# Optimization experiments

Measured on AMD Instinct MI355X. Metric: run time of the kernel, lower is better.

The kernel has to match this reference:

```python
import jax, jax.numpy as jnp
import numpy as np

VOCAB, EMB = 100000, 50
KERNEL_NUM, SIGMA, EXACT_SIGMA = 21, 0.1, 0.001
OUT_LAYERS = [10, 5]


def _kernel_params():
    # Mirrors KNRM._get_kernels_layers
    mus = [1.0]
    bin_size = 2.0 / (KERNEL_NUM - 1)
    mus.append(1 - bin_size / 2)
    for i in range(1, KERNEL_NUM - 1):
        mus.append(mus[i] - bin_size)
    mus = list(reversed(mus))
    sigmas = [SIGMA] * (KERNEL_NUM - 1) + [EXACT_SIGMA]
    return np.array(mus, np.float32), np.array(sigmas, np.float32)

MUS, SIGMAS = _kernel_params()


def setup_inputs() -> dict:
    key = jax.random.key(0)
    ks = jax.random.split(key, 12)
    B, LQ, LD = 2048, 32, 256
    emb = jax.random.normal(ks[0], (VOCAB, EMB), jnp.float32)
    emb = emb.at[0].set(0.0)  # padding_idx=0
    query1 = jax.random.randint(ks[1], (B, LQ), 0, VOCAB)
    doc1 = jax.random.randint(ks[2], (B, LD), 0, VOCAB)
    query2 = jax.random.randint(ks[3], (B, LQ), 0, VOCAB)
    doc2 = jax.random.randint(ks[4], (B, LD), 0, VOCAB)
    def lin(k, fan_in, fan_out):
        bound = 1.0 / np.sqrt(fan_in)
        kw, kb = jax.random.split(k)
        w = jax.random.uniform(kw, (fan_out, fan_in), jnp.float32, -bound, bound)
        b = jax.random.uniform(kb, (fan_out,), jnp.float32, -bound, bound)
        return w, b
    w0, b0 = lin(ks[5], KERNEL_NUM, OUT_LAYERS[0])
    w1, b1 = lin(ks[6], OUT_LAYERS[0], OUT_LAYERS[1])
    w2, b2 = lin(ks[7], OUT_LAYERS[1], 1)
    return dict(emb=emb, w0=w0, b0=b0, w1=w1, b1=b1, w2=w2, b2=b2,
                query1=query1, doc1=doc1, query2=query2, doc2=doc2)


def _matching_matrix(emb, query, doc):
    qe = emb[query]                     # [B, Lq, E]
    de = emb[doc]                       # [B, Ld, E]
    qn = qe / (jnp.linalg.norm(qe, axis=-1, keepdims=True) + 1e-13)
    dn = de / (jnp.linalg.norm(de, axis=-1, keepdims=True) + 1e-13)
    return jnp.einsum('bqe,bde->bqd', qn, dn)  # cosine sim [B, Lq, Ld]


def _apply_kernels(mm):
    # Loop over the fixed 21 kernels (structurally distinct mu/sigma),
    # avoiding a [B,Lq,Ld,21] intermediate, as the original does.
    km = []
    for mu, sg in zip(MUS, SIGMAS):
        k = jnp.exp(-(mm - mu) ** 2 / (2.0 * sg * sg))
        km.append(jnp.log1p(k.sum(axis=-1)).sum(axis=-1))  # [B]
    return jnp.stack(km, axis=1)  # [B, K]


def _mlp(x, w0, b0, w1, b1, w2, b2):
    h = jax.nn.relu(x @ w0.T + b0)
    h = jax.nn.relu(h @ w1.T + b1)
    return h @ w2.T + b2  # [B, 1]


def _predict(emb, w0, b0, w1, b1, w2, b2, query, doc):
    mm = _matching_matrix(emb, query, doc)
    ko = _apply_kernels(mm)
    return _mlp(ko, w0, b0, w1, b1, w2, b2)


def reference(emb, w0, b0, w1, b1, w2, b2, query1, doc1, query2, doc2):
    logits1 = _predict(emb, w0, b0, w1, b1, w2, b2, query1, doc1)
    logits2 = _predict(emb, w0, b0, w1, b1, w2, b2, query2, doc2)
    return jax.nn.sigmoid(logits1 - logits2)  # [B, 1]
```

## Files before the change

### kernel.cpp

```cpp
#include <hip/hip_runtime.h>

#define EMB_N 50
#define KP 64
#define LQ 32
#define LD 256
#define KN 21
#define BATCH 2048

typedef short v8s __attribute__((ext_vector_type(8)));
typedef float v4f __attribute__((ext_vector_type(4)));
typedef float v2f __attribute__((ext_vector_type(2)));

#define PK_ACC(d, b)    asm("v_pk_add_f32 %0, %0, %1" : "+v"(d) : "v"(b))
#define PK_MULA(d, b)   asm("v_pk_mul_f32 %0, %0, %1" : "+v"(d) : "v"(b))

__device__ inline short bf16_rne(float f) {
  unsigned u = __float_as_uint(f);
  unsigned r = u + 0x7fffu + ((u >> 16) & 1u);
  return (short)(r >> 16);
}
__device__ inline float bf16_tof(short h) {
  return __uint_as_float(((unsigned)(unsigned short)h) << 16);
}

__global__ __launch_bounds__(256) void vocab_norm_kernel(
    const float* __restrict__ emb, short* __restrict__ vb,
    short* __restrict__ vlo, int vocab)
{
  int gid = blockIdx.x * 256 + threadIdx.x;
  int r = gid >> 3;
  int c = gid & 7;
  if (r >= vocab) return;
  const float* row = emb + (size_t)r * EMB_N;
  float v[8];
#pragma unroll
  for (int k = 0; k < 8; k++) v[k] = 0.f;
  float ss = 0.f;
  int e0 = c * 8;
  if (c < 6) {
    const float2* p = (const float2*)(row + e0);
#pragma unroll
    for (int k = 0; k < 4; k++) {
      float2 t = p[k];
      v[2*k] = t.x; v[2*k+1] = t.y;
      ss = fmaf(t.x, t.x, ss); ss = fmaf(t.y, t.y, ss);
    }
  } else if (c == 6) {
    float2 t = *(const float2*)(row + 48);
    v[0] = t.x; v[1] = t.y;
    ss = fmaf(t.x, t.x, t.y * t.y);
  }
  ss += __shfl_xor(ss, 1);
  ss += __shfl_xor(ss, 2);
  ss += __shfl_xor(ss, 4);
  float inv = 1.0f / (sqrtf(ss) + 1e-13f);
  short hi[8], lo[8];
#pragma unroll
  for (int k = 0; k < 8; k++) {
    float f = v[k] * inv;
    hi[k] = bf16_rne(f);
    lo[k] = bf16_rne(f - bf16_tof(hi[k]));
  }
  size_t o = (size_t)r * KP + e0;
  *(uint4*)(vb + o)  = *(const uint4*)hi;
  *(uint4*)(vlo + o) = *(const uint4*)lo;
}

__device__ __constant__ const float CJ[KN] = {
  2.5261639e-20f, 2.0469719e-16f, 6.1019363e-13f, 6.6915861e-10f, 2.6995785e-7f,
  4.0065297e-5f,  2.1874911e-3f,  4.3936937e-2f,  0.32465247f,    0.88249690f,
  0.88249690f,    0.32465247f,    4.3936937e-2f,  2.1874911e-3f,  4.0065297e-5f,
  2.6995785e-7f,  6.6915861e-10f, 6.1019363e-13f, 2.0469719e-16f, 2.5261639e-20f,
  1.0f
};

__global__ __launch_bounds__(256, 6) void knrm_main_kernel(
    const short* __restrict__ vb, const short* __restrict__ vlo,
    const int* __restrict__ q1, const int* __restrict__ d1,
    const int* __restrict__ q2, const int* __restrict__ d2,
    const float* __restrict__ w0, const float* __restrict__ b0,
    const float* __restrict__ w1, const float* __restrict__ b1,
    const float* __restrict__ w2, const float* __restrict__ b2,
    float* __restrict__ lgbuf)
{
  __shared__ float part[4][16][KN];
  __shared__ float Sqex[LQ];
  __shared__ float ko[KN];
  __shared__ float h0s[10];
  __shared__ float h1s[5];

  const int pair = blockIdx.x >> 11;
  const int b = blockIdx.x & (BATCH - 1);
  const int tid = threadIdx.x;
  const int wave = tid >> 6;
  const int lane = tid & 63;
  const int l15 = lane & 15;
  const int quad = lane >> 4;
  const int qtile = wave >> 1;
  const int thalf = wave & 1;

  const int* qp = pair ? q2 : q1;
  const int* dp = pair ? d2 : d1;

  if (tid < LQ) Sqex[tid] = 0.f;

  int qtok = qp[b * LQ + qtile * 16 + l15];
  const short* qh = vb  + (size_t)qtok * KP + quad * 8;
  const short* ql = vlo + (size_t)qtok * KP + quad * 8;
  v8s Bh0 = *(const v8s*)(qh);
  v8s Bh1 = *(const v8s*)(qh + 32);
  v8s Bl0 = *(const v8s*)(ql);
  v8s Bl1 = *(const v8s*)(ql + 32);

  int mydtok = dp[b * LD + tid];

  __syncthreads();

#pragma unroll
  for (int qq = 0; qq < LQ; qq++) {
    int qt = qp[b * LQ + qq];
    unsigned long long m = __ballot(mydtok == qt && qt != 0);
    if (lane == 0 && m)
      atomicAdd(&Sqex[qq], (float)__popcll(m));
  }

  v2f U2[10];
#pragma unroll
  for (int i = 0; i < 10; i++) U2[i] = (v2f){0.f, 0.f};

#pragma unroll 1
  for (int t = 0; t < 8; t++) {
    int dtok = dp[b * LD + (thalf * 8 + t) * 16 + l15];
    const short* dptr = vb + (size_t)dtok * KP + quad * 8;
    v8s A0 = *(const v8s*)(dptr);
    v8s A1 = *(const v8s*)(dptr + 32);

    v4f C = {0.f, 0.f, 0.f, 0.f};
    C = __builtin_amdgcn_mfma_f32_16x16x32_bf16(A0, Bh0, C, 0, 0, 0);
    C = __builtin_amdgcn_mfma_f32_16x16x32_bf16(A1, Bh1, C, 0, 0, 0);
    C = __builtin_amdgcn_mfma_f32_16x16x32_bf16(A0, Bl0, C, 0, 0, 0);
    C = __builtin_amdgcn_mfma_f32_16x16x32_bf16(A1, Bl1, C, 0, 0, 0);

#pragma unroll
    for (int rp = 0; rp < 2; rp++) {
      v2f p0, p1, rr0, rr1;
      {
        float x = C[rp * 2];
        float gc = __builtin_amdgcn_exp2f(x * fmaf(-72.1347520f, x, 7.2134752f));
        float ex = 14.4269504f * x;
        float e1 = __builtin_amdgcn_exp2f(ex);
        float ei = __builtin_amdgcn_exp2f(-ex);
        p0 = (v2f){gc, gc * ei};  rr0 = (v2f){e1, ei};
      }
      {
        float x = C[rp * 2 + 1];
        float gc = __builtin_amdgcn_exp2f(x * fmaf(-72.1347520f, x, 7.2134752f));
        float ex = 14.4269504f * x;
        float e1 = __builtin_amdgcn_exp2f(ex);
        float ei = __builtin_amdgcn_exp2f(-ex);
        p1 = (v2f){gc, gc * ei};  rr1 = (v2f){e1, ei};
      }
#pragma unroll
      for (int k2 = 0; k2 < 10; k2++) {
        PK_ACC(U2[k2], p0);
        PK_MULA(p0, rr0);
        PK_ACC(U2[k2], p1);
        PK_MULA(p1, rr1);
      }
    }
  }

#pragma unroll
  for (int i = 0; i < 10; i++) {
    float ux = U2[i].x, uy = U2[i].y;
    ux += __shfl_xor(ux, 16);  uy += __shfl_xor(uy, 16);
    ux += __shfl_xor(ux, 32);  uy += __shfl_xor(uy, 32);
    if (quad == 0) {
      part[wave][l15][10 + i] = ux;
      part[wave][l15][9 - i]  = uy;
    }
  }
  __syncthreads();

  {
    int qq = tid & 31;
    int qi = qq & 15, qt2 = qq >> 4;
    int jb = tid >> 5;
#pragma unroll
    for (int k = 0; k < 3; k++) {
      int j = jb + 8 * k;
      float l = 0.f;
      if (j < KN) {
        float s = (j < 20) ? part[qt2 * 2][qi][j] + part[qt2 * 2 + 1][qi][j]
                           : Sqex[qq];
        float y = fmaf(CJ[j], s, 1.0f);
        l = 0.69314718f * __builtin_amdgcn_logf(y);
      }
      l += __shfl_xor(l, 1);  l += __shfl_xor(l, 2);
      l += __shfl_xor(l, 4);  l += __shfl_xor(l, 8);
      l += __shfl_xor(l, 16);
      if (qq == 0 && j < KN) ko[j] = l;
    }
  }
  __syncthreads();

  if (tid < 10) {
    float h = b0[tid];
#pragma unroll
    for (int k = 0; k < KN; k++) h = fmaf(w0[tid * KN + k], ko[k], h);
    h0s[tid] = fmaxf(h, 0.f);
  }
  __syncthreads();
  if (tid < 5) {
    float h = b1[tid];
#pragma unroll
    for (int k = 0; k < 10; k++) h = fmaf(w1[tid * 10 + k], h0s[k], h);
    h1s[tid] = fmaxf(h, 0.f);
  }
  __syncthreads();
  if (tid == 0) {
    float h = b2[0];
#pragma unroll
    for (int k = 0; k < 5; k++) h = fmaf(w2[k], h1s[k], h);
    lgbuf[pair * BATCH + b] = h;
  }
}

__global__ __launch_bounds__(256) void knrm_combine_kernel(
    const float* __restrict__ lgbuf, float* __restrict__ out)
{
  int i = blockIdx.x * 256 + threadIdx.x;
  if (i < BATCH) {
    float z = lgbuf[i] - lgbuf[BATCH + i];
    out[i] = 1.0f / (1.0f + expf(-z));
  }
}

extern "C" void kernel_launch(void* const* d_in, const int* in_sizes, int n_in,
                              void* d_out, int out_size, void* d_ws, size_t ws_size,
                              hipStream_t stream)
{
  const float* emb = (const float*)d_in[0];
  const float* w0  = (const float*)d_in[1];
  const float* b0  = (const float*)d_in[2];
  const float* w1  = (const float*)d_in[3];
  const float* b1  = (const float*)d_in[4];
  const float* w2  = (const float*)d_in[5];
  const float* b2  = (const float*)d_in[6];
  const int* q1 = (const int*)d_in[7];
  const int* dd1 = (const int*)d_in[8];
  const int* q2 = (const int*)d_in[9];
  const int* dd2 = (const int*)d_in[10];
  float* out = (float*)d_out;

  int vocab = in_sizes[0] / EMB_N;
  int B = in_sizes[7] / LQ;

  float* lgbuf = (float*)d_ws;
  short* vb  = (short*)(lgbuf + 2 * BATCH);
  short* vlo = vb + (size_t)vocab * KP;

  vocab_norm_kernel<<<(vocab * 8 + 255) / 256, 256, 0, stream>>>(emb, vb, vlo, vocab);
  knrm_main_kernel<<<2 * B, 256, 0, stream>>>(vb, vlo, q1, dd1, q2, dd2,
                                              w0, b0, w1, b1, w2, b2, lgbuf);
  knrm_combine_kernel<<<(B + 255) / 256, 256, 0, stream>>>(lgbuf, out);
}
```

Measured before the change: 143.9 us.

## Stage vocab rows through LDS and fuse sigmoid combine into main kernel

The vocab normalisation kernel now loads 64 embedding rows per block into shared memory with coalesced float4 reads, then normalises them from LDS, in place of strided float2 global reads. The separate combine kernel is removed. The second of the two blocks for a batch item computes the sigmoid, using an atomic counter per batch entry and release/acquire on the logits. This saves one kernel launch and makes the embedding reads coalesced, but adds a memset, atomics, and a per-row serial loop over LDS.

After: 327.5 us. 2.28x slower.

```diff
diff --git a/kernel.cpp b/kernel.cpp
--- a/kernel.cpp
+++ b/kernel.cpp
@@ -6,6 +6,7 @@
 #define LD 256
 #define KN 21
 #define BATCH 2048
+#define VROWS 64
 
 typedef short v8s __attribute__((ext_vector_type(8)));
 typedef float v4f __attribute__((ext_vector_type(4)));
@@ -23,32 +24,49 @@
   return __uint_as_float(((unsigned)(unsigned short)h) << 16);
 }
 
-__global__ __launch_bounds__(256) void vocab_norm_kernel(
+__global__ __launch_bounds__(512) void vocab_norm_kernel(
     const float* __restrict__ emb, short* __restrict__ vb,
     short* __restrict__ vlo, int vocab)
 {
-  int gid = blockIdx.x * 256 + threadIdx.x;
-  int r = gid >> 3;
-  int c = gid & 7;
-  if (r >= vocab) return;
-  const float* row = emb + (size_t)r * EMB_N;
+  __shared__ float lds[VROWS * EMB_N];
+  const int tid = threadIdx.x;
+  const long long ftotal = (long long)vocab * EMB_N;
+  const long long fbase  = (long long)blockIdx.x * (VROWS * EMB_N);
+
+  const float4* e4 = (const float4*)emb;
+#pragma unroll
+  for (int i = 0; i < 2; i++) {
+    int idx = i * 512 + tid;
+    if (idx < (VROWS * EMB_N) / 4) {
+      long long g4 = fbase / 4 + idx;
+      if (g4 * 4 + 3 < ftotal) {
+        *(float4*)&lds[idx * 4] = e4[g4];
+      } else {
+#pragma unroll
+        for (int k = 0; k < 4; k++) {
+          long long gf = g4 * 4 + k;
+          lds[idx * 4 + k] = (gf < ftotal) ? emb[gf] : 0.f;
+        }
+      }
+    }
+  }
+  __syncthreads();
+
+  const int r = tid >> 3;
+  const int c = tid & 7;
+  const int row = blockIdx.x * VROWS + r;
+  if (row >= vocab) return;
+
   float v[8];
 #pragma unroll
   for (int k = 0; k < 8; k++) v[k] = 0.f;
   float ss = 0.f;
-  int e0 = c * 8;
-  if (c < 6) {
-    const float2* p = (const float2*)(row + e0);
-#pragma unroll
-    for (int k = 0; k < 4; k++) {
-      float2 t = p[k];
-      v[2*k] = t.x; v[2*k+1] = t.y;
-      ss = fmaf(t.x, t.x, ss); ss = fmaf(t.y, t.y, ss);
-    }
-  } else if (c == 6) {
-    float2 t = *(const float2*)(row + 48);
-    v[0] = t.x; v[1] = t.y;
-    ss = fmaf(t.x, t.x, t.y * t.y);
+  const int e0 = c * 8;
+  const int cnt = (c < 6) ? 8 : (c == 6 ? 2 : 0);
+  for (int k = 0; k < cnt; k++) {
+    float t = lds[r * EMB_N + e0 + k];
+    v[k] = t;
+    ss = fmaf(t, t, ss);
   }
   ss += __shfl_xor(ss, 1);
   ss += __shfl_xor(ss, 2);
@@ -61,7 +79,7 @@
     hi[k] = bf16_rne(f);
     lo[k] = bf16_rne(f - bf16_tof(hi[k]));
   }
-  size_t o = (size_t)r * KP + e0;
+  size_t o = (size_t)row * KP + e0;
   *(uint4*)(vb + o)  = *(const uint4*)hi;
   *(uint4*)(vlo + o) = *(const uint4*)lo;
 }
@@ -81,7 +99,8 @@
     const float* __restrict__ w0, const float* __restrict__ b0,
     const float* __restrict__ w1, const float* __restrict__ b1,
     const float* __restrict__ w2, const float* __restrict__ b2,
-    float* __restrict__ lgbuf)
+    float* __restrict__ lgbuf, int* __restrict__ flags,
+    float* __restrict__ out)
 {
   __shared__ float part[4][16][KN];
   __shared__ float Sqex[LQ];
@@ -222,17 +241,16 @@
     float h = b2[0];
 #pragma unroll
     for (int k = 0; k < 5; k++) h = fmaf(w2[k], h1s[k], h);
-    lgbuf[pair * BATCH + b] = h;
-  }
-}
-
-__global__ __launch_bounds__(256) void knrm_combine_kernel(
-    const float* __restrict__ lgbuf, float* __restrict__ out)
-{
-  int i = blockIdx.x * 256 + threadIdx.x;
-  if (i < BATCH) {
-    float z = lgbuf[i] - lgbuf[BATCH + i];
-    out[i] = 1.0f / (1.0f + expf(-z));
+    __hip_atomic_store(&lgbuf[pair * BATCH + b], h,
+                       __ATOMIC_RELEASE, __HIP_MEMORY_SCOPE_AGENT);
+    int old = __hip_atomic_fetch_add(&flags[b], 1,
+                                     __ATOMIC_ACQ_REL, __HIP_MEMORY_SCOPE_AGENT);
+    if (old == 1) {
+      float other = __hip_atomic_load(&lgbuf[(1 - pair) * BATCH + b],
+                                      __ATOMIC_ACQUIRE, __HIP_MEMORY_SCOPE_AGENT);
+      float z = pair ? (other - h) : (h - other);
+      out[b] = 1.0f / (1.0f + __expf(-z));
+    }
   }
 }
 
@@ -257,11 +275,13 @@
   int B = in_sizes[7] / LQ;
 
   float* lgbuf = (float*)d_ws;
-  short* vb  = (short*)(lgbuf + 2 * BATCH);
+  int*   flags = (int*)(lgbuf + 2 * BATCH);
+  short* vb  = (short*)(flags + BATCH);
   short* vlo = vb + (size_t)vocab * KP;
 
-  vocab_norm_kernel<<<(vocab * 8 + 255) / 256, 256, 0, stream>>>(emb, vb, vlo, vocab);
+  hipMemsetAsync(flags, 0, BATCH * sizeof(int), stream);
+  vocab_norm_kernel<<<(vocab + VROWS - 1) / VROWS, 512, 0, stream>>>(emb, vb, vlo, vocab);
   knrm_main_kernel<<<2 * B, 256, 0, stream>>>(vb, vlo, q1, dd1, q2, dd2,
-                                              w0, b0, w1, b1, w2, b2, lgbuf);
-  knrm_combine_kernel<<<(B + 255) / 256, 256, 0, stream>>>(lgbuf, out);
-}
+                                              w0, b0, w1, b1, w2, b2,
+                                              lgbuf, flags, out);
+}
```
